# Optimization experiments

Hardware: AMD Instinct MI355X
Metric: run time of the kernel (lower is better)

The kernel has to match this reference:

```python
import jax, jax.numpy as jnp
import numpy as np

ENT_SIZE = 100000; REL_SIZE = 500; ENT_DIM = 256; REL_DIM = 256; H = 256
E = 2048; S = 32; N = 1024; THRESHOLD = 1.0; EPS = 1e-5


def _xav(k, shape):
    fan_in = shape[-1]
    fan_out = shape[-2] if len(shape) > 1 else shape[-1]
    std = (2.0 / (fan_in + fan_out)) ** 0.5
    return jax.random.normal(k, shape, jnp.float32) * std


def setup_inputs() -> dict:
    key = jax.random.key(0)
    ks = jax.random.split(key, 16)
    inp = {}
    inp["neighbors"] = jax.random.randint(ks[0], (E, S), 0, ENT_SIZE)
    inp["pos_h"] = jax.random.randint(ks[1], (N,), 0, E)
    inp["pos_t"] = jax.random.randint(ks[2], (N,), 0, E)
    inp["pos_r"] = jax.random.randint(ks[3], (N,), 0, REL_SIZE)
    inp["neg_h"] = jax.random.randint(ks[4], (N,), 0, E)
    inp["neg_t"] = jax.random.randint(ks[5], (N,), 0, E)
    inp["neg_r"] = jax.random.randint(ks[6], (N,), 0, REL_SIZE)
    inp["ent_embed"] = _xav(ks[7], (ENT_SIZE + 1, ENT_DIM))
    inp["rel_embed"] = _xav(ks[8], (REL_SIZE, REL_DIM))
    inp["trans"] = _xav(ks[9], (2 * REL_SIZE, REL_DIM, ENT_DIM))
    inp["W_ih_f"] = _xav(ks[10], (4 * H, ENT_DIM)); inp["W_hh_f"] = _xav(ks[11], (4 * H, H))
    inp["W_ih_b"] = _xav(ks[12], (4 * H, ENT_DIM)); inp["W_hh_b"] = _xav(ks[13], (4 * H, H))
    inp["b_f"] = jnp.zeros((4 * H,), jnp.float32)
    inp["b_b"] = jnp.zeros((4 * H,), jnp.float32)
    inp["W_lin"] = _xav(ks[14], (ENT_DIM, 2 * H)); inp["b_lin"] = jnp.zeros((ENT_DIM,), jnp.float32)
    inp["gamma"] = jnp.ones((ENT_DIM,), jnp.float32); inp["beta"] = jnp.zeros((ENT_DIM,), jnp.float32)
    return inp


def _lstm_final(x, W_ih, W_hh, b):
    # x: [E,S,D] -> final hidden state [E,H] (PyTorch LSTM gate order i,f,g,o; b = b_ih+b_hh)
    h0 = jnp.zeros((x.shape[0], H), x.dtype)
    def step(carry, xt):
        h, c = carry
        g = xt @ W_ih.T + h @ W_hh.T + b  # [E,4H]
        i, f, gg, o = jnp.split(g, 4, axis=-1)
        c = jax.nn.sigmoid(f) * c + jax.nn.sigmoid(i) * jnp.tanh(gg)
        h = jax.nn.sigmoid(o) * jnp.tanh(c)
        return (h, c), None
    (h, _), _ = jax.lax.scan(step, (h0, h0), jnp.swapaxes(x, 0, 1))
    return h


def _context(ent_embed, neighbors, W_ih_f, W_hh_f, b_f, W_ih_b, W_hh_b, b_b, W_lin, b_lin, gamma, beta):
    x_seq = ent_embed[neighbors]  # [E,S,D]
    h_f = _lstm_final(x_seq, W_ih_f, W_hh_f, b_f)
    h_b = _lstm_final(x_seq[:, ::-1], W_ih_b, W_hh_b, b_b)
    lin = jnp.concatenate([h_f, h_b], -1) @ W_lin.T + b_lin  # [E,ENT_DIM]
    # BatchNorm1d in training mode: batch stats (biased variance)
    mu = lin.mean(0)
    var = lin.var(0)
    return jnp.tanh(gamma * (lin - mu) * jax.lax.rsqrt(var + EPS) + beta)


def _score(trans, rel_embed, ctx, h_idx, r_idx, t_idx):
    Wh = trans[r_idx]             # [N,REL_DIM,ENT_DIM] (grouped expert GEMV, batched)
    Wt = trans[r_idx + REL_SIZE]
    d = jnp.einsum('nre,ne->nr', Wh, ctx[h_idx]) - jnp.einsum('nre,ne->nr', Wt, ctx[t_idx])
    return jnp.linalg.norm(d + rel_embed[r_idx], axis=1)


def reference(neighbors, pos_h, pos_t, pos_r, neg_h, neg_t, neg_r,
              ent_embed, rel_embed, trans, W_ih_f, W_hh_f, W_ih_b, W_hh_b,
              b_f, b_b, W_lin, b_lin, gamma, beta):
    ctx = _context(ent_embed, neighbors, W_ih_f, W_hh_f, b_f, W_ih_b, W_hh_b, b_b,
                   W_lin, b_lin, gamma, beta)
    pos_n = _score(trans, rel_embed, ctx, pos_h, pos_r, pos_t)
    neg_n = _score(trans, rel_embed, ctx, neg_h, neg_r, neg_t)
    return jnp.sum(pos_n + jax.nn.relu(THRESHOLD - neg_n))
```

## Files before the change

kernel.cpp:

```cpp
#include <hip/hip_runtime.h>

constexpr int kE   = 2048;
constexpr int kS   = 32;
constexpr int kD   = 256;
constexpr int kK   = 512;
constexpr int kREL = 500;
constexpr int kN   = 1024;

typedef unsigned short u16;
typedef __attribute__((ext_vector_type(8))) _Float16 f16x8;
typedef __attribute__((ext_vector_type(4))) float    f32x4;
typedef __attribute__((ext_vector_type(4))) unsigned short us4;

static __device__ __forceinline__ u16 f2h(float f) {
  _Float16 h = (_Float16)f;
  return __builtin_bit_cast(u16, h);
}
static __device__ __forceinline__ float h2f(u16 v) {
  _Float16 h = __builtin_bit_cast(_Float16, v);
  return (float)h;
}
static __device__ __forceinline__ float sigf(float x) { return 1.f / (1.f + __expf(-x)); }
static __device__ __forceinline__ float tanhfast(float x) {
  float e = __expf(2.f * x);
  return 1.f - 2.f / (e + 1.f);
}

__global__ void prep_weights(const float* __restrict__ Wih_f, const float* __restrict__ Whh_f,
                             const float* __restrict__ Wih_b, const float* __restrict__ Whh_b,
                             const float* __restrict__ Wlin_in,
                             u16* __restrict__ Wihr, u16* __restrict__ Whhr,
                             u16* __restrict__ Wlin) {
  int idx = blockIdx.x * 256 + threadIdx.x;
  if (idx < 65536) {
    int d = idx >> 15;
    int j = (idx & 32767) >> 5;
    int k = (idx & 31) * 8;
    int g = (j >> 4) & 3, u = (j >> 6) * 16 + (j & 15);
    int R = g * 256 + u;
    const float* src = (d ? Wih_b : Wih_f) + R * 256 + k;
    ushort oa[8];
#pragma unroll
    for (int i = 0; i < 8; i++) oa[i] = f2h(src[i]);
    *(uint4*)((char*)Wihr + (size_t)idx * 16) = *(uint4*)oa;
  } else if (idx < 131072) {
    int i2 = idx - 65536;
    int d = i2 >> 15;
    int j = (i2 & 32767) >> 5;
    int k = (i2 & 31) * 8;
    int g = (j >> 4) & 3, u = (j >> 6) * 16 + (j & 15);
    int R = g * 256 + u;
    const float* src = (d ? Whh_b : Whh_f) + R * 256 + k;
    ushort oa[8];
#pragma unroll
    for (int i = 0; i < 8; i++) oa[i] = f2h(src[i]);
    *(uint4*)((char*)Whhr + (size_t)i2 * 16) = *(uint4*)oa;
  } else if (idx < 131072 + 16384) {
    int q = (idx - 131072) * 8;
#pragma unroll
    for (int i = 0; i < 8; i++) Wlin[q + i] = f2h(Wlin_in[q + i]);
  }
}

__global__ void gather_x(const int* __restrict__ neighbors, const float* __restrict__ ent,
                         u16* __restrict__ x16) {
  const int tot = kS * kE * kD / 4;
  for (int i = blockIdx.x * blockDim.x + threadIdx.x; i < tot; i += gridDim.x * blockDim.x) {
    int k4 = i & 63;
    int row = i >> 6;
    int e = row & (kE - 1);
    int s = row >> 11;
    int nb = neighbors[e * kS + s];
    float4 v = *(const float4*)(ent + (size_t)nb * kD + k4 * 4);
    ushort4 o;
    o.x = f2h(v.x); o.y = f2h(v.y); o.z = f2h(v.z); o.w = f2h(v.w);
    *(ushort4*)(x16 + (size_t)row * kD + k4 * 4) = o;
  }
}

__global__ __launch_bounds__(256) void xgemm(
    const u16* __restrict__ x16, const u16* __restrict__ Wihr,
    const float* __restrict__ b_f, const float* __restrict__ b_b,
    u16* __restrict__ gx, int t0, int T) {
  __shared__ __align__(16) char smem[40960];
  u16* As = (u16*)smem;
  u16* Bs = (u16*)(smem + 8192);
  const int tid = threadIdx.x, lane = tid & 63, w = tid >> 6;
  const int l15 = lane & 15, lq = lane >> 4;
  const int row0 = blockIdx.x * 64;
  const int y = blockIdx.y;
  const int dir = blockIdx.z;
  const int tt = row0 >> 11;
  const int e0 = row0 & 2047;
  const int s = dir ? (31 - (t0 + tt)) : (t0 + tt);
  const u16* Ab = x16 + ((size_t)s * kE + e0) * kD;
  const u16* Bb = Wihr + ((size_t)dir * 1024 + y * 256) * kD;
  const float* bd = dir ? b_b : b_f;
  const int u = (y * 4 + w) * 16 + l15;
  float bb4[4];
#pragma unroll
  for (int n = 0; n < 4; n++) bb4[n] = bd[n * 256 + u];

  f32x4 acc[4][4];
#pragma unroll
  for (int m = 0; m < 4; m++)
#pragma unroll
    for (int n = 0; n < 4; n++) acc[m][n] = (f32x4){0.f, 0.f, 0.f, 0.f};

  for (int ch = 0; ch < 4; ++ch) {
    const int k0 = ch * 64;
    __syncthreads();
#pragma unroll
    for (int i = 0; i < 2; i++) {
      int idx = tid + i * 256;
      int row = idx >> 3, c8 = idx & 7;
      uint4 v = *(const uint4*)(Ab + (size_t)row * kD + k0 + c8 * 8);
      *(uint4*)((char*)As + row * 128 + ((c8 * 16) ^ ((row & 7) << 4))) = v;
    }
#pragma unroll
    for (int i = 0; i < 8; i++) {
      int idx = tid + i * 256;
      int j = idx >> 3, c8 = idx & 7;
      uint4 v = *(const uint4*)(Bb + (size_t)j * kD + k0 + c8 * 8);
      *(uint4*)((char*)Bs + j * 128 + ((c8 * 16) ^ ((j & 7) << 4))) = v;
    }
    __syncthreads();
#pragma unroll
    for (int ks = 0; ks < 2; ++ks) {
      const int kb = ks * 64 + lq * 16;
      f16x8 a[4], b[4];
#pragma unroll
      for (int m = 0; m < 4; m++) {
        int row = m * 16 + l15;
        a[m] = *(const f16x8*)((const char*)As + row * 128 + (kb ^ ((row & 7) << 4)));
      }
#pragma unroll
      for (int n = 0; n < 4; n++) {
        int row = w * 64 + n * 16 + l15;
        b[n] = *(const f16x8*)((const char*)Bs + row * 128 + (kb ^ ((row & 7) << 4)));
      }
#pragma unroll
      for (int m = 0; m < 4; m++)
#pragma unroll
        for (int n = 0; n < 4; n++)
          acc[m][n] = __builtin_amdgcn_mfma_f32_16x16x32_f16(a[m], b[n], acc[m][n], 0, 0, 0);
    }
  }

  u16* out = gx + (((size_t)dir * T + tt) * kE) * 1024;
#pragma unroll
  for (int m = 0; m < 4; m++)
#pragma unroll
    for (int r = 0; r < 4; r++) {
      int e = e0 + m * 16 + lq * 4 + r;
      us4 o;
      o[0] = f2h(acc[m][0][r] + bb4[0]); o[1] = f2h(acc[m][1][r] + bb4[1]);
      o[2] = f2h(acc[m][2][r] + bb4[2]); o[3] = f2h(acc[m][3][r] + bb4[3]);
      __builtin_nontemporal_store(o, (us4*)(out + ((size_t)e * 256 + u) * 4));
    }
}

__global__ __launch_bounds__(256) void lstm_step(
    const u16* __restrict__ gx, const u16* __restrict__ Whhr,
    const u16* __restrict__ hprev, u16* __restrict__ hnext,
    float* __restrict__ cbuf, int tt, int T) {
  const int tid = threadIdx.x, lane = tid & 63, w = tid >> 6;
  const int l15 = lane & 15, lq = lane >> 4;
  const int bid = blockIdx.x;
  const int dir = bid >> 7;
  const int ut  = (bid >> 4) & 7;
  const int et  = bid & 15;
  const int wr = w >> 1, wc = w & 1;
  const int e0 = et * 128 + wr * 64;
  const int c0 = ut * 128 + wc * 64;
  const int unit = (c0 >> 6) * 16 + l15;

  const u16* Wd  = Whhr + (size_t)dir * 1024 * kD;
  const u16* hpd = hprev + (size_t)dir * kE * kD;
  u16* hnd = hnext + (size_t)dir * kE * kD;
  float* cd = cbuf + (size_t)dir * kE * kD;
  const u16* gp = gx + ((size_t)dir * T + tt) * kE * 1024;

  f32x4 acc[4][4];
#pragma unroll
  for (int m = 0; m < 4; m++)
#pragma unroll
    for (int r = 0; r < 4; r++) {
      us4 g = __builtin_nontemporal_load(
          (const us4*)(gp + (size_t)(e0 + m * 16 + lq * 4 + r) * 1024 + unit * 4));
#pragma unroll
      for (int n = 0; n < 4; n++) acc[m][n][r] = h2f(g[n]);
    }

  const int klane = lq * 8;
#pragma unroll
  for (int ks = 0; ks < 8; ks++) {
    const int ka = ks * 32 + klane;
    f16x8 a[4], b[4];
#pragma unroll
    for (int m = 0; m < 4; m++)
      a[m] = *(const f16x8*)(hpd + (size_t)(e0 + m * 16 + l15) * kD + ka);
#pragma unroll
    for (int n = 0; n < 4; n++)
      b[n] = *(const f16x8*)(Wd + (size_t)(c0 + n * 16 + l15) * kD + ka);
#pragma unroll
    for (int m = 0; m < 4; m++)
#pragma unroll
      for (int n = 0; n < 4; n++)
        acc[m][n] = __builtin_amdgcn_mfma_f32_16x16x32_f16(a[m], b[n], acc[m][n], 0, 0, 0);
  }

#pragma unroll
  for (int m = 0; m < 4; m++)
#pragma unroll
    for (int r = 0; r < 4; r++) {
      int row = e0 + m * 16 + lq * 4 + r;
      size_t off = (size_t)row * kD + unit;
      float gi = acc[m][0][r];
      float gf = acc[m][1][r];
      float gg = acc[m][2][r];
      float go = acc[m][3][r];
      float c_old = cd[off];
      float cn = sigf(gf) * c_old + sigf(gi) * tanhfast(gg);
      cd[off] = cn;
      hnd[off] = f2h(sigf(go) * tanhfast(cn));
    }
}

static __device__ __forceinline__ void gemm_tile(
    const u16* __restrict__ Alo, const u16* __restrict__ Ahi,
    const u16* __restrict__ W, int e0,
    u16* As, u16* Bs, f32x4 (&acc)[4][4]) {
  const int tid = threadIdx.x;
  const int lane = tid & 63;
  const int w = tid >> 6;
#pragma unroll
  for (int m = 0; m < 4; m++)
#pragma unroll
    for (int n = 0; n < 4; n++) acc[m][n] = (f32x4){0.f, 0.f, 0.f, 0.f};

  for (int ch = 0; ch < 8; ++ch) {
    const int k0 = ch * 64;
    __syncthreads();
    const u16* Asrc = (k0 < 256) ? Alo : Ahi;
    const int kbase = (k0 < 256) ? k0 : (k0 - 256);
#pragma unroll
    for (int i = 0; i < 2; i++) {
      int idx = tid + i * 256;
      int row = idx >> 3, c8 = idx & 7;
      uint4 v = *(const uint4*)(Asrc + (size_t)(e0 + row) * 256 + kbase + c8 * 8);
      *(uint4*)((char*)As + row * 128 + ((c8 * 16) ^ ((row & 7) << 4))) = v;
    }
#pragma unroll
    for (int i = 0; i < 8; i++) {
      int idx = tid + i * 256;
      int j = idx >> 3, c8 = idx & 7;
      uint4 v = *(const uint4*)(W + (size_t)j * kK + k0 + c8 * 8);
      *(uint4*)((char*)Bs + j * 128 + ((c8 * 16) ^ ((j & 7) << 4))) = v;
    }
    __syncthreads();
#pragma unroll
    for (int ks = 0; ks < 2; ++ks) {
      const int kb = ks * 64 + (lane >> 4) * 16;
      f16x8 a[4], b[4];
#pragma unroll
      for (int m = 0; m < 4; m++) {
        int row = m * 16 + (lane & 15);
        a[m] = *(const f16x8*)((const char*)As + row * 128 + (kb ^ ((row & 7) << 4)));
      }
#pragma unroll
      for (int n = 0; n < 4; n++) {
        int row = w * 64 + n * 16 + (lane & 15);
        b[n] = *(const f16x8*)((const char*)Bs + row * 128 + (kb ^ ((row & 7) << 4)));
      }
#pragma unroll
      for (int m = 0; m < 4; m++)
#pragma unroll
        for (int n = 0; n < 4; n++)
          acc[m][n] = __builtin_amdgcn_mfma_f32_16x16x32_f16(a[m], b[n], acc[m][n], 0, 0, 0);
    }
  }
}

__global__ __launch_bounds__(256) void lin_kernel(
    const u16* __restrict__ hf, const u16* __restrict__ hb,
    const u16* __restrict__ Wl, const float* __restrict__ b_lin,
    float* __restrict__ lin) {
  __shared__ __align__(16) char smem[40960];
  u16* As = (u16*)smem;
  u16* Bs = (u16*)(smem + 8192);
  const int tid = threadIdx.x, lane = tid & 63, w = tid >> 6;
  const int e0 = blockIdx.x * 64;
  f32x4 acc[4][4];
  gemm_tile(hf, hb, Wl, e0, As, Bs, acc);
#pragma unroll
  for (int m = 0; m < 4; m++)
#pragma unroll
    for (int n = 0; n < 4; n++)
#pragma unroll
      for (int r = 0; r < 4; r++) {
        int e = e0 + m * 16 + (lane >> 4) * 4 + r;
        int col = w * 64 + n * 16 + (lane & 15);
        lin[(size_t)e * 256 + col] = acc[m][n][r] + b_lin[col];
      }
}

__global__ void bn_stats(const float* __restrict__ lin, float* __restrict__ part) {
  int b = blockIdx.x, c = threadIdx.x;
  float s = 0.f, s2 = 0.f;
  for (int e = b * 32; e < b * 32 + 32; ++e) {
    float x = lin[(size_t)e * 256 + c];
    s += x; s2 += x * x;
  }
  part[b * 256 + c] = s;
  part[64 * 256 + b * 256 + c] = s2;
}

__global__ void bn_apply(const float* __restrict__ lin, const float* __restrict__ part,
                         const float* __restrict__ gamma, const float* __restrict__ beta,
                         float* __restrict__ ctx) {
  int c = threadIdx.x;
  float s = 0.f, s2 = 0.f;
  for (int b = 0; b < 64; b++) { s += part[b * 256 + c]; s2 += part[64 * 256 + b * 256 + c]; }
  float mu = s * (1.f / 2048.f);
  float rsig = rsqrtf(s2 * (1.f / 2048.f) - mu * mu + 1e-5f);
  float ga = gamma[c], be = beta[c];
  int e0 = blockIdx.x * 8;
  for (int e = e0; e < e0 + 8; ++e) {
    float x = lin[(size_t)e * 256 + c];
    ctx[(size_t)e * 256 + c] = tanhf(ga * (x - mu) * rsig + be);
  }
}

__global__ void group_rel(const int* __restrict__ pr, const int* __restrict__ nr,
                          int* __restrict__ offs, int* __restrict__ list) {
  __shared__ int cnt[512], sc[512], cur[512];
  int tid = threadIdx.x;
  cnt[tid] = 0;
  __syncthreads();
  for (int i = tid; i < 2 * kN; i += 512) {
    int r = (i < kN) ? pr[i] : nr[i - kN];
    atomicAdd(&cnt[r], 1);
  }
  __syncthreads();
  sc[tid] = cnt[tid];
  __syncthreads();
  for (int d = 1; d < 512; d <<= 1) {
    int v = (tid >= d) ? sc[tid - d] : 0;
    __syncthreads();
    sc[tid] += v;
    __syncthreads();
  }
  int excl = (tid == 0) ? 0 : sc[tid - 1];
  cur[tid] = excl;
  if (tid <= kREL) offs[tid] = excl;
  __syncthreads();
  for (int i = tid; i < 2 * kN; i += 512) {
    int r = (i < kN) ? pr[i] : nr[i - kN];
    int p = atomicAdd(&cur[r], 1);
    list[p] = i;
  }
}

__global__ __launch_bounds__(256) void score_grouped(
    const float* __restrict__ ctx, const float* __restrict__ trans,
    const float* __restrict__ rel_embed,
    const int* __restrict__ ph, const int* __restrict__ pt,
    const int* __restrict__ nh, const int* __restrict__ nt,
    const int* __restrict__ offs, const int* __restrict__ list,
    float* __restrict__ scores) {
  int r = blockIdx.x;
  int start = offs[r], end = offs[r + 1];
  if (start >= end) return;
  int tid = threadIdx.x;
  __shared__ float cs[8][2][256];
  __shared__ float red[8][4];
  float relv = rel_embed[r * 256 + tid];
  const float4* Whp = (const float4*)(trans + (size_t)r * 65536 + (size_t)tid * 256);
  const float4* Wtp = (const float4*)(trans + ((size_t)r + kREL) * 65536 + (size_t)tid * 256);

  for (int chunk = start; chunk < end; chunk += 8) {
    int G = min(8, end - chunk);
    for (int j = 0; j < G; j++) {
      int i = list[chunk + j];
      int hh = (i < kN) ? ph[i] : nh[i - kN];
      int tt = (i < kN) ? pt[i] : nt[i - kN];
      cs[j][0][tid] = ctx[(size_t)hh * 256 + tid];
      cs[j][1][tid] = ctx[(size_t)tt * 256 + tid];
    }
    __syncthreads();
    float acc[8];
#pragma unroll
    for (int j = 0; j < 8; j++) acc[j] = relv;
#pragma unroll 2
    for (int q = 0; q < 64; q++) {
      float4 w1 = Whp[q];
      float4 w2 = Wtp[q];
#pragma unroll
      for (int j = 0; j < 8; j++) {
        float4 xh = *(const float4*)&cs[j][0][q * 4];
        float4 xt = *(const float4*)&cs[j][1][q * 4];
        acc[j] += w1.x * xh.x + w1.y * xh.y + w1.z * xh.z + w1.w * xh.w
                - (w2.x * xt.x + w2.y * xt.y + w2.z * xt.z + w2.w * xt.w);
      }
    }
    for (int j = 0; j < G; j++) {
      float sq = acc[j] * acc[j];
      for (int o = 32; o; o >>= 1) sq += __shfl_down(sq, o);
      if ((tid & 63) == 0) red[j][tid >> 6] = sq;
    }
    __syncthreads();
    if (tid < G) {
      float s = red[tid][0] + red[tid][1] + red[tid][2] + red[tid][3];
      scores[list[chunk + tid]] = sqrtf(s);
    }
    __syncthreads();
  }
}

__global__ void final_reduce(const float* __restrict__ scores, float* __restrict__ out) {
  int tid = threadIdx.x;
  float a = 0.f;
  for (int i = tid; i < 2 * kN; i += 256) {
    float s = scores[i];
    a += (i < kN) ? s : fmaxf(0.f, 1.f - s);
  }
  for (int off = 32; off; off >>= 1) a += __shfl_down(a, off);
  __shared__ float w4[4];
  if ((tid & 63) == 0) w4[tid >> 6] = a;
  __syncthreads();
  if (tid == 0) out[0] = w4[0] + w4[1] + w4[2] + w4[3];
}

extern "C" void kernel_launch(void* const* d_in, const int* in_sizes, int n_in,
                              void* d_out, int out_size, void* d_ws, size_t ws_size,
                              hipStream_t stream) {
  const int*   neighbors = (const int*)d_in[0];
  const int*   pos_h = (const int*)d_in[1];
  const int*   pos_t = (const int*)d_in[2];
  const int*   pos_r = (const int*)d_in[3];
  const int*   neg_h = (const int*)d_in[4];
  const int*   neg_t = (const int*)d_in[5];
  const int*   neg_r = (const int*)d_in[6];
  const float* ent_embed = (const float*)d_in[7];
  const float* rel_embed = (const float*)d_in[8];
  const float* trans = (const float*)d_in[9];
  const float* W_ih_f = (const float*)d_in[10];
  const float* W_hh_f = (const float*)d_in[11];
  const float* W_ih_b = (const float*)d_in[12];
  const float* W_hh_b = (const float*)d_in[13];
  const float* b_f = (const float*)d_in[14];
  const float* b_b = (const float*)d_in[15];
  const float* W_lin = (const float*)d_in[16];
  const float* b_lin = (const float*)d_in[17];
  const float* gamma = (const float*)d_in[18];
  const float* beta = (const float*)d_in[19];

  char* ws = (char*)d_ws;
  size_t off = 0;
  auto alloc = [&](size_t bytes) {
    void* p = ws + off;
    off = (off + bytes + 255) & ~(size_t)255;
    return p;
  };
  u16* Wihr   = (u16*)alloc((size_t)2 * 1024 * kD * 2);
  u16* Whhr   = (u16*)alloc((size_t)2 * 1024 * kD * 2);
  u16* Wlin   = (u16*)alloc((size_t)256 * kK * 2);
  u16* x16    = (u16*)alloc((size_t)kS * kE * kD * 2);
  u16* h0     = (u16*)alloc((size_t)2 * kE * kD * 2);
  u16* h1     = (u16*)alloc((size_t)2 * kE * kD * 2);
  float* cbuf = (float*)alloc((size_t)2 * kE * kD * 4);
  float* lin  = (float*)alloc((size_t)kE * 256 * 4);
  float* part = (float*)alloc((size_t)2 * 64 * 256 * 4);
  float* ctx  = (float*)alloc((size_t)kE * 256 * 4);
  float* scores = (float*)alloc((size_t)2 * kN * 4);
  int* offsb  = (int*)alloc((size_t)512 * 4);
  int* list   = (int*)alloc((size_t)2 * kN * 4);
  size_t fixed_end = off;
  (void)in_sizes; (void)n_in; (void)out_size;

  int T = 2;
  for (int cand = 32; cand >= 2; cand >>= 1) {
    size_t gxb = (size_t)2 * cand * kE * 1024 * 2;
    if (fixed_end + gxb + (1 << 20) <= ws_size) { T = cand; break; }
  }
  u16* gx = (u16*)alloc((size_t)2 * T * kE * 1024 * 2);

  hipMemsetAsync(h0, 0, (size_t)2 * kE * kD * 2, stream);
  hipMemsetAsync(cbuf, 0, (size_t)2 * kE * kD * 4, stream);

  prep_weights<<<576, 256, 0, stream>>>(W_ih_f, W_hh_f, W_ih_b, W_hh_b, W_lin,
                                        Wihr, Whhr, Wlin);
  gather_x<<<4096, 256, 0, stream>>>(neighbors, ent_embed, x16);
  group_rel<<<1, 512, 0, stream>>>(pos_r, neg_r, offsb, list);

  for (int t0 = 0; t0 < kS; t0 += T) {
    xgemm<<<dim3(T * 32, 4, 2), 256, 0, stream>>>(x16, Wihr, b_f, b_b, gx, t0, T);
    for (int tt = 0; tt < T; tt++) {
      int t = t0 + tt;
      const u16* hp = (t & 1) ? h1 : h0;
      u16* hn = (t & 1) ? h0 : h1;
      lstm_step<<<256, 256, 0, stream>>>(gx, Whhr, hp, hn, cbuf, tt, T);
    }
  }

  lin_kernel<<<32, 256, 0, stream>>>(h0, h0 + (size_t)kE * kD, Wlin, b_lin, lin);
  bn_stats<<<64, 256, 0, stream>>>(lin, part);
  bn_apply<<<256, 256, 0, stream>>>(lin, part, gamma, beta, ctx);
  score_grouped<<<kREL, 256, 0, stream>>>(ctx, trans, rel_embed,
                                          pos_h, pos_t, neg_h, neg_t, offsb, list, scores);
  final_reduce<<<1, 256, 0, stream>>>(scores, (float*)d_out);
}
```

Measured before the change: 825.2 us.

## Drop LDS staging in xgemm and split lstm_step into smaller tiles

xgemm now loads A and B fragments straight from global memory into MFMA registers instead of staging them through swizzled shared memory, and seeds the accumulators with the bias. This removes the barriers and the LDS round-trip, but relies on the cache for reuse across waves. lstm_step now uses 32-row by 256-unit tiles per block with 512 blocks instead of 256, which puts more blocks on the many CUs of the chip for the latency-bound recurrent step. Each wave now reads 4 weight fragments for only 2 row fragments, so more weight traffic is issued per MFMA.

After: 951.6 us. 15.3% more time.

```diff
diff --git a/kernel.cpp b/kernel.cpp
--- a/kernel.cpp
+++ b/kernel.cpp
@@ -82,9 +82,6 @@
     const u16* __restrict__ x16, const u16* __restrict__ Wihr,
     const float* __restrict__ b_f, const float* __restrict__ b_b,
     u16* __restrict__ gx, int t0, int T) {
-  __shared__ __align__(16) char smem[40960];
-  u16* As = (u16*)smem;
-  u16* Bs = (u16*)(smem + 8192);
   const int tid = threadIdx.x, lane = tid & 63, w = tid >> 6;
   const int l15 = lane & 15, lq = lane >> 4;
   const int row0 = blockIdx.x * 64;
@@ -94,57 +91,35 @@
   const int e0 = row0 & 2047;
   const int s = dir ? (31 - (t0 + tt)) : (t0 + tt);
   const u16* Ab = x16 + ((size_t)s * kE + e0) * kD;
-  const u16* Bb = Wihr + ((size_t)dir * 1024 + y * 256) * kD;
+  const int c0 = y * 256 + w * 64;
+  const u16* Bb = Wihr + ((size_t)dir * 1024 + c0) * kD;
   const float* bd = dir ? b_b : b_f;
-  const int u = (y * 4 + w) * 16 + l15;
-  float bb4[4];
-#pragma unroll
-  for (int n = 0; n < 4; n++) bb4[n] = bd[n * 256 + u];
+  const int u = (c0 >> 6) * 16 + l15;
 
   f32x4 acc[4][4];
 #pragma unroll
-  for (int m = 0; m < 4; m++)
-#pragma unroll
-    for (int n = 0; n < 4; n++) acc[m][n] = (f32x4){0.f, 0.f, 0.f, 0.f};
-
-  for (int ch = 0; ch < 4; ++ch) {
-    const int k0 = ch * 64;
-    __syncthreads();
-#pragma unroll
-    for (int i = 0; i < 2; i++) {
-      int idx = tid + i * 256;
-      int row = idx >> 3, c8 = idx & 7;
-      uint4 v = *(const uint4*)(Ab + (size_t)row * kD + k0 + c8 * 8);
-      *(uint4*)((char*)As + row * 128 + ((c8 * 16) ^ ((row & 7) << 4))) = v;
-    }
-#pragma unroll
-    for (int i = 0; i < 8; i++) {
-      int idx = tid + i * 256;
-      int j = idx >> 3, c8 = idx & 7;
-      uint4 v = *(const uint4*)(Bb + (size_t)j * kD + k0 + c8 * 8);
-      *(uint4*)((char*)Bs + j * 128 + ((c8 * 16) ^ ((j & 7) << 4))) = v;
-    }
-    __syncthreads();
-#pragma unroll
-    for (int ks = 0; ks < 2; ++ks) {
-      const int kb = ks * 64 + lq * 16;
-      f16x8 a[4], b[4];
-#pragma unroll
-      for (int m = 0; m < 4; m++) {
-        int row = m * 16 + l15;
-        a[m] = *(const f16x8*)((const char*)As + row * 128 + (kb ^ ((row & 7) << 4)));
-      }
-#pragma unroll
-      for (int n = 0; n < 4; n++) {
-        int row = w * 64 + n * 16 + l15;
-        b[n] = *(const f16x8*)((const char*)Bs + row * 128 + (kb ^ ((row & 7) << 4)));
-      }
-#pragma unroll
-      for (int m = 0; m < 4; m++)
-#pragma unroll
-        for (int n = 0; n < 4; n++)
-          acc[m][n] = __builtin_amdgcn_mfma_f32_16x16x32_f16(a[m], b[n], acc[m][n], 0, 0, 0);
-    }
+  for (int n = 0; n < 4; n++) {
+    float bv = bd[n * 256 + u];
+#pragma unroll
+    for (int m = 0; m < 4; m++) acc[m][n] = (f32x4){bv, bv, bv, bv};
+  }
+
+  const int klane = lq * 8;
+#pragma unroll
+  for (int ks = 0; ks < 8; ks++) {
+    const int ka = ks * 32 + klane;
+    f16x8 a[4], b[4];
+#pragma unroll
+    for (int m = 0; m < 4; m++)
+      a[m] = *(const f16x8*)(Ab + (size_t)(m * 16 + l15) * kD + ka);
+#pragma unroll
+    for (int n = 0; n < 4; n++)
+      b[n] = *(const f16x8*)(Bb + (size_t)(n * 16 + l15) * kD + ka);
+#pragma unroll
+    for (int m = 0; m < 4; m++)
+#pragma unroll
+      for (int n = 0; n < 4; n++)
+        acc[m][n] = __builtin_amdgcn_mfma_f32_16x16x32_f16(a[m], b[n], acc[m][n], 0, 0, 0);
   }
 
   u16* out = gx + (((size_t)dir * T + tt) * kE) * 1024;
@@ -154,8 +129,8 @@
     for (int r = 0; r < 4; r++) {
       int e = e0 + m * 16 + lq * 4 + r;
       us4 o;
-      o[0] = f2h(acc[m][0][r] + bb4[0]); o[1] = f2h(acc[m][1][r] + bb4[1]);
-      o[2] = f2h(acc[m][2][r] + bb4[2]); o[3] = f2h(acc[m][3][r] + bb4[3]);
+      o[0] = f2h(acc[m][0][r]); o[1] = f2h(acc[m][1][r]);
+      o[2] = f2h(acc[m][2][r]); o[3] = f2h(acc[m][3][r]);
       __builtin_nontemporal_store(o, (us4*)(out + ((size_t)e * 256 + u) * 4));
     }
 }
@@ -167,23 +142,23 @@
   const int tid = threadIdx.x, lane = tid & 63, w = tid >> 6;
   const int l15 = lane & 15, lq = lane >> 4;
   const int bid = blockIdx.x;
-  const int dir = bid >> 7;
-  const int ut  = (bid >> 4) & 7;
-  const int et  = bid & 15;
-  const int wr = w >> 1, wc = w & 1;
-  const int e0 = et * 128 + wr * 64;
-  const int c0 = ut * 128 + wc * 64;
+  const int dir = bid >> 8;
+  const int rem = bid & 255;
+  const int jg = rem >> 6;
+  const int et = rem & 63;
+  const int e0 = et * 32;
+  const int c0 = jg * 256 + w * 64;
   const int unit = (c0 >> 6) * 16 + l15;
 
-  const u16* Wd  = Whhr + (size_t)dir * 1024 * kD;
+  const u16* Wd  = Whhr + ((size_t)dir * 1024 + c0) * kD;
   const u16* hpd = hprev + (size_t)dir * kE * kD;
   u16* hnd = hnext + (size_t)dir * kE * kD;
   float* cd = cbuf + (size_t)dir * kE * kD;
   const u16* gp = gx + ((size_t)dir * T + tt) * kE * 1024;
 
-  f32x4 acc[4][4];
-#pragma unroll
-  for (int m = 0; m < 4; m++)
+  f32x4 acc[2][4];
+#pragma unroll
+  for (int m = 0; m < 2; m++)
 #pragma unroll
     for (int r = 0; r < 4; r++) {
       us4 g = __builtin_nontemporal_load(
@@ -196,22 +171,22 @@
 #pragma unroll
   for (int ks = 0; ks < 8; ks++) {
     const int ka = ks * 32 + klane;
-    f16x8 a[4], b[4];
-#pragma unroll
-    for (int m = 0; m < 4; m++)
+    f16x8 a[2], b[4];
+#pragma unroll
+    for (int m = 0; m < 2; m++)
       a[m] = *(const f16x8*)(hpd + (size_t)(e0 + m * 16 + l15) * kD + ka);
 #pragma unroll
     for (int n = 0; n < 4; n++)
-      b[n] = *(const f16x8*)(Wd + (size_t)(c0 + n * 16 + l15) * kD + ka);
-#pragma unroll
-    for (int m = 0; m < 4; m++)
+      b[n] = *(const f16x8*)(Wd + (size_t)(n * 16 + l15) * kD + ka);
+#pragma unroll
+    for (int m = 0; m < 2; m++)
 #pragma unroll
       for (int n = 0; n < 4; n++)
         acc[m][n] = __builtin_amdgcn_mfma_f32_16x16x32_f16(a[m], b[n], acc[m][n], 0, 0, 0);
   }
 
 #pragma unroll
-  for (int m = 0; m < 4; m++)
+  for (int m = 0; m < 2; m++)
 #pragma unroll
     for (int r = 0; r < 4; r++) {
       int row = e0 + m * 16 + lq * 4 + r;
@@ -500,7 +475,7 @@
       int t = t0 + tt;
       const u16* hp = (t & 1) ? h1 : h0;
       u16* hn = (t & 1) ? h0 : h1;
-      lstm_step<<<256, 256, 0, stream>>>(gx, Whhr, hp, hn, cbuf, tt, T);
+      lstm_step<<<512, 256, 0, stream>>>(gx, Whhr, hp, hn, cbuf, tt, T);
     }
   }
 
```
